# Performance work log

Hardware: AMD Instinct MI355X
Metric: run time of the kernel (lower is better)

## Reference

```python
import jax, jax.numpy as jnp
import numpy as np
import math

PHI = (1.0 + math.sqrt(5.0)) / 2.0
B, S, E, H = 4, 1024, 1024, 16
D = E // H  # head_dim = 64


def setup_inputs() -> dict:
    key = jax.random.key(0)
    ks = jax.random.split(key, 16)
    w = 0.02  # stand-in for xavier(gain=1/phi); math is init-agnostic
    inp = {
        "query": jax.random.normal(ks[0], (B, S, E), jnp.float32),
        "key": jax.random.normal(ks[1], (B, S, E), jnp.float32),
        "value": jax.random.normal(ks[2], (B, S, E), jnp.float32),
        "consciousness_levels": jax.random.uniform(ks[3], (B, S), jnp.float32),
        # causal mask, broadcast over batch and heads
        "attn_mask": jnp.tril(jnp.ones((S, S), bool))[None, None],
        # projection weights stored [in, out] (torch Linear applies x @ W.T)
        "Wq": jax.random.normal(ks[4], (E, E), jnp.float32) * w,
        "bq": jnp.zeros((E,), jnp.float32),
        "Wk": jax.random.normal(ks[5], (E, E), jnp.float32) * w,
        "bk": jnp.zeros((E,), jnp.float32),
        "Wv": jax.random.normal(ks[6], (E, E), jnp.float32) * w,
        "bv": jnp.zeros((E,), jnp.float32),
        "Wo": jax.random.normal(ks[7], (E, E), jnp.float32) * w,
        "bo": jnp.zeros((E,), jnp.float32),
        "Wc": jax.random.normal(ks[8], (E, H), jnp.float32) * w,
        "bc": jnp.zeros((H,), jnp.float32),
        # phi_bias[h] = (h+1)/phi**(h+1), shape [H,1,1] as in _init_weights
        "phi_bias": jnp.array([(h + 1) / PHI ** (h + 1) for h in range(H)],
                               jnp.float32).reshape(H, 1, 1),
    }
    return inp


def reference(query, key, value, consciousness_levels, attn_mask,
              Wq, bq, Wk, bk, Wv, bv, Wo, bo, Wc, bc, phi_bias):
    # project and split heads: [B,S,E] -> [B,H,S,D]
    q = (query @ Wq + bq).reshape(B, S, H, D).transpose(0, 2, 1, 3)
    k = (key @ Wk + bk).reshape(B, S, H, D).transpose(0, 2, 1, 3)
    v = (value @ Wv + bv).reshape(B, S, H, D).transpose(0, 2, 1, 3)

    inv_scale = 1.0 / (math.sqrt(D) * math.sqrt(PHI))  # phi-scaled 1/sqrt(d)
    scores = jnp.einsum('bhqd,bhkd->bhqk', q, k) * inv_scale
    scores = scores + phi_bias[None]                   # per-head additive bias
    scores = jnp.where(attn_mask, scores, -jnp.inf)
    attn = jax.nn.softmax(scores, axis=-1)             # [B,H,S,S]

    # consciousness reweighting + second softmax (faithful to original)
    cw = jax.nn.softmax(query @ Wc + bc, axis=-1)      # [B,S,H]
    cw = cw.transpose(0, 2, 1)[..., None]              # [B,H,S,1]
    cb = consciousness_levels[:, None, :, None]        # [B,1,S,1]
    attn = jax.nn.softmax(attn * (1.0 + cb * cw), axis=-1)

    ctx = jnp.einsum('bhqk,bhkd->bhqd', attn, v)
    ctx = ctx.transpose(0, 2, 1, 3).reshape(B, S, E)
    out = ctx @ Wo + bo
    return out, attn
```

## Files before the change

kernel.cpp:

```cpp
#include <hip/hip_runtime.h>
#include <stdint.h>

#define B_ 4
#define S_ 1024
#define E_ 1024
#define H_ 16
#define D_ 64

typedef unsigned short u16;
typedef short s16x8 __attribute__((ext_vector_type(8)));
typedef unsigned short u16x8 __attribute__((ext_vector_type(8)));
typedef unsigned short u16x4 __attribute__((ext_vector_type(4)));
typedef float f32x4 __attribute__((ext_vector_type(4)));

__device__ __forceinline__ u16 f2bf(float f) {
    union { float f; uint32_t i; } x; x.f = f;
    uint32_t r = (x.i + 0x7FFFu + ((x.i >> 16) & 1u)) >> 16;
    return (u16)r;
}

__device__ __forceinline__ float wave_sum(float v) {
    #pragma unroll
    for (int o = 32; o; o >>= 1) v += __shfl_xor(v, o);
    return v;
}

template<int BM, int BN, int EPI, bool AF32>
__global__ __launch_bounds__(256, 2)
void gemm_bt(const void* __restrict__ Avoid, int lda, long sA,
             const u16* __restrict__ BT, int ldb, long sB,
             const float* __restrict__ bias,
             void* __restrict__ Cvoid, int ldc, int K)
{
    constexpr int BK = 32;
    constexpr int FM = BM / 32;
    constexpr int FN = BN / 32;
    constexpr int NAF = (BM * BK) / 4 / 256;
    constexpr int NAB = (BM * BK) / 8 / 256;
    constexpr int NB  = (BN * BK) / 8 / 256;
    __shared__ __attribute__((aligned(16))) u16 As[BM * BK];
    __shared__ __attribute__((aligned(16))) u16 Bs[BN * BK];

    const int t = threadIdx.x;
    const int lane = t & 63;
    const int wave = t >> 6;
    const int wr = wave >> 1, wc = wave & 1;
    const int z = blockIdx.z;
    const int m0 = blockIdx.y * BM, n0 = blockIdx.x * BN;

    const float* Af = ((const float*)Avoid) + (size_t)z * sA;
    const u16*  Ab  = ((const u16*)Avoid) + (size_t)z * sA;
    const u16*  Bp  = BT + (size_t)z * sB;

    f32x4 ra[NAF];
    u16x8 rab[NAB];
    u16x8 rb[NB];

    auto loadA = [&](int k0) {
        if constexpr (AF32) {
            #pragma unroll
            for (int i = 0; i < NAF; i++) {
                int c = i * 256 + t, row = c >> 3, cc = c & 7;
                ra[i] = *(const f32x4*)(Af + (size_t)(m0 + row) * lda + k0 + cc * 4);
            }
        } else {
            #pragma unroll
            for (int i = 0; i < NAB; i++) {
                int c = i * 256 + t, row = c >> 2, cc = c & 3;
                rab[i] = *(const u16x8*)(Ab + (size_t)(m0 + row) * lda + k0 + cc * 8);
            }
        }
    };
    auto loadB = [&](int k0) {
        #pragma unroll
        for (int i = 0; i < NB; i++) {
            int c = i * 256 + t, row = c >> 2, cc = c & 3;
            rb[i] = *(const u16x8*)(Bp + (size_t)(n0 + row) * ldb + k0 + cc * 8);
        }
    };
    auto storeLDS = [&]() {
        if constexpr (AF32) {
            #pragma unroll
            for (int i = 0; i < NAF; i++) {
                int c = i * 256 + t;
                u16x4 o;
                o[0] = f2bf(ra[i][0]); o[1] = f2bf(ra[i][1]);
                o[2] = f2bf(ra[i][2]); o[3] = f2bf(ra[i][3]);
                *(u16x4*)(As + c * 4) = o;
            }
        } else {
            #pragma unroll
            for (int i = 0; i < NAB; i++) {
                int c = i * 256 + t;
                *(u16x8*)(As + c * 8) = rab[i];
            }
        }
        #pragma unroll
        for (int i = 0; i < NB; i++) {
            int c = i * 256 + t;
            *(u16x8*)(Bs + c * 8) = rb[i];
        }
    };

    f32x4 acc[FM][FN];
    #pragma unroll
    for (int i = 0; i < FM; i++)
        #pragma unroll
        for (int j = 0; j < FN; j++)
            acc[i][j] = (f32x4){0.f, 0.f, 0.f, 0.f};

    const int al = lane & 15;
    const int aq = lane >> 4;

    loadA(0); loadB(0);
    for (int k0 = 0; k0 < K; k0 += BK) {
        __syncthreads();
        storeLDS();
        __syncthreads();
        if (k0 + BK < K) { loadA(k0 + BK); loadB(k0 + BK); }

        s16x8 af[FM], bf[FN];
        #pragma unroll
        for (int i = 0; i < FM; i++)
            af[i] = *(const s16x8*)(As + ((wr * FM + i) * 16 + al) * BK + aq * 8);
        #pragma unroll
        for (int j = 0; j < FN; j++)
            bf[j] = *(const s16x8*)(Bs + ((wc * FN + j) * 16 + al) * BK + aq * 8);
        #pragma unroll
        for (int i = 0; i < FM; i++)
            #pragma unroll
            for (int j = 0; j < FN; j++)
                acc[i][j] = __builtin_amdgcn_mfma_f32_16x16x32_bf16(af[i], bf[j], acc[i][j], 0, 0, 0);
    }

    float* Cf = (float*)Cvoid;
    u16*   Cb = (u16*)Cvoid;
    #pragma unroll
    for (int i = 0; i < FM; i++) {
        #pragma unroll
        for (int j = 0; j < FN; j++) {
            const int col = n0 + (wc * FN + j) * 16 + al;
            const float bv = bias[col];
            #pragma unroll
            for (int r = 0; r < 4; r++) {
                const int row = m0 + (wr * FM + i) * 16 + aq * 4 + r;
                float v = acc[i][j][r] + bv;
                if (EPI == 0) {
                    Cf[(size_t)row * ldc + col] = v;
                } else if (EPI == 1) {
                    int b = row >> 10, s = row & 1023, h = col >> 6, d = col & 63;
                    Cb[((size_t)((b * H_ + h) * S_ + s)) * D_ + d] = f2bf(v);
                } else {
                    int b = row >> 10, s = row & 1023, h = col >> 6, d = col & 63;
                    Cb[((size_t)((b * H_ + h) * D_ + d)) * S_ + s] = f2bf(v);
                }
            }
        }
    }
}

__global__ __launch_bounds__(256)
void cons_k(const float* __restrict__ query, const float* __restrict__ Wc,
            const float* __restrict__ bc, const float* __restrict__ cl,
            float* __restrict__ mws)
{
    const int t = threadIdx.x, lane = t & 63, wave = t >> 6;
    const int r = blockIdx.x * 4 + wave;
    const float* qrow = query + (size_t)r * E_;
    float acc[H_];
    #pragma unroll
    for (int c = 0; c < H_; c++) acc[c] = 0.f;
    for (int e = lane; e < E_; e += 64) {
        float qv = qrow[e];
        const float* wp = Wc + e * H_;
        f32x4 w0 = *(const f32x4*)(wp);
        f32x4 w1 = *(const f32x4*)(wp + 4);
        f32x4 w2 = *(const f32x4*)(wp + 8);
        f32x4 w3 = *(const f32x4*)(wp + 12);
        #pragma unroll
        for (int c = 0; c < 4; c++) {
            acc[c]      += qv * w0[c];
            acc[4 + c]  += qv * w1[c];
            acc[8 + c]  += qv * w2[c];
            acc[12 + c] += qv * w3[c];
        }
    }
    #pragma unroll
    for (int c = 0; c < H_; c++) acc[c] = wave_sum(acc[c]);
    float mx = -3e38f;
    #pragma unroll
    for (int c = 0; c < H_; c++) { acc[c] += bc[c]; mx = fmaxf(mx, acc[c]); }
    float se = 0.f;
    #pragma unroll
    for (int c = 0; c < H_; c++) { acc[c] = __expf(acc[c] - mx); se += acc[c]; }
    if (lane < H_) {
        float mycw = 0.f;
        #pragma unroll
        for (int c = 0; c < H_; c++) if (lane == c) mycw = acc[c];
        mycw /= se;
        int b = r >> 10, s = r & 1023;
        float clv = cl[r];
        mws[((size_t)(b * H_ + lane)) * S_ + s] = 1.f + clv * mycw;
    }
}

#define LD_ 1028
__global__ __launch_bounds__(256, 2)
void attn_fused(const u16* __restrict__ q_ws, const u16* __restrict__ k_ws,
                const u16* __restrict__ vt_ws, const float* __restrict__ mws,
                float* __restrict__ attn_out, u16* __restrict__ ctx_ws,
                float alpha)
{
    __shared__ __attribute__((aligned(16))) float sc[16 * LD_];
    __shared__ float red[16 * 16];
    __shared__ float rowmax[16], scl1[16], invz[16];

    const int t = threadIdx.x, lane = t & 63, w = t >> 6;
    const int al = lane & 15, aq = lane >> 4;
    const int bh = blockIdx.y;
    const int q0 = blockIdx.x * 16;

    const u16* Qp = q_ws + ((size_t)bh * S_ + q0) * D_;
    const u16* Kp = k_ws + (size_t)bh * S_ * D_ + (size_t)(w * 256) * D_;
    const u16* Vp = vt_ws + (size_t)bh * D_ * S_;

    s16x8 qf0 = *(const s16x8*)(Qp + (size_t)al * D_ + aq * 8);
    s16x8 qf1 = *(const s16x8*)(Qp + (size_t)al * D_ + 32 + aq * 8);
    #pragma unroll
    for (int mf = 0; mf < 16; mf++) {
        const u16* kr = Kp + (size_t)(mf * 16 + al) * D_ + aq * 8;
        s16x8 kf0 = *(const s16x8*)(kr);
        s16x8 kf1 = *(const s16x8*)(kr + 32);
        f32x4 a0 = (f32x4){0.f, 0.f, 0.f, 0.f};
        a0 = __builtin_amdgcn_mfma_f32_16x16x32_bf16(kf0, qf0, a0, 0, 0, 0);
        a0 = __builtin_amdgcn_mfma_f32_16x16x32_bf16(kf1, qf1, a0, 0, 0, 0);
        const int kc = w * 256 + mf * 16 + aq * 4;
        f32x4 o;
        #pragma unroll
        for (int j = 0; j < 4; j++) o[j] = a0[j] * alpha;
        *(f32x4*)(sc + (size_t)al * LD_ + kc) = o;
    }
    __syncthreads();

    const int row = t & 15, cg = t >> 4;
    const int q = q0 + row;
    float* rp = sc + (size_t)row * LD_ + cg * 4;

    float mx = -3e38f;
    #pragma unroll 4
    for (int k = 0; k < 16; k++) {
        f32x4 v = *(const f32x4*)(rp + k * 64);
        const int cb = cg * 4 + k * 64;
        #pragma unroll
        for (int j = 0; j < 4; j++)
            if (cb + j <= q) mx = fmaxf(mx, v[j]);
    }
    red[cg * 16 + row] = mx;
    __syncthreads();
    if (t < 16) {
        float m = red[t];
        #pragma unroll
        for (int c = 1; c < 16; c++) m = fmaxf(m, red[c * 16 + t]);
        rowmax[t] = m;
    }
    __syncthreads();

    const float mxr = rowmax[row];
    float s1 = 0.f;
    #pragma unroll 4
    for (int k = 0; k < 16; k++) {
        f32x4 v = *(const f32x4*)(rp + k * 64);
        const int cb = cg * 4 + k * 64;
        f32x4 o;
        #pragma unroll
        for (int j = 0; j < 4; j++) {
            float e = (cb + j <= q) ? __expf(v[j] - mxr) : 0.f;
            o[j] = e; s1 += e;
        }
        *(f32x4*)(rp + k * 64) = o;
    }
    red[cg * 16 + row] = s1;
    __syncthreads();
    if (t < 16) {
        float s = 0.f;
        #pragma unroll
        for (int c = 0; c < 16; c++) s += red[c * 16 + t];
        scl1[t] = mws[(size_t)bh * S_ + q0 + t] / s;
    }
    __syncthreads();

    const float sl = scl1[row];
    float s2 = 0.f;
    #pragma unroll 4
    for (int k = 0; k < 16; k++) {
        f32x4 v = *(const f32x4*)(rp + k * 64);
        const int cb = cg * 4 + k * 64;
        f32x4 o;
        #pragma unroll
        for (int j = 0; j < 4; j++) {
            float e = (cb + j <= q) ? __expf(v[j] * sl) : 1.f;
            o[j] = e; s2 += e;
        }
        *(f32x4*)(rp + k * 64) = o;
    }
    red[cg * 16 + row] = s2;
    __syncthreads();
    if (t < 16) {
        float s = 0.f;
        #pragma unroll
        for (int c = 0; c < 16; c++) s += red[c * 16 + t];
        invz[t] = 1.f / s;
    }
    __syncthreads();

    f32x4 pa[4];
    #pragma unroll
    for (int nf = 0; nf < 4; nf++) pa[nf] = (f32x4){0.f, 0.f, 0.f, 0.f};
    #pragma unroll
    for (int ks = 0; ks < 8; ks++) {
        const int kb = w * 256 + ks * 32;
        const float* ap = sc + (size_t)al * LD_ + kb + aq * 8;
        f32x4 x0 = *(const f32x4*)(ap);
        f32x4 x1 = *(const f32x4*)(ap + 4);
        s16x8 af;
        af[0] = (short)f2bf(x0[0]); af[1] = (short)f2bf(x0[1]);
        af[2] = (short)f2bf(x0[2]); af[3] = (short)f2bf(x0[3]);
        af[4] = (short)f2bf(x1[0]); af[5] = (short)f2bf(x1[1]);
        af[6] = (short)f2bf(x1[2]); af[7] = (short)f2bf(x1[3]);
        #pragma unroll
        for (int nf = 0; nf < 4; nf++) {
            s16x8 bf = *(const s16x8*)(Vp + (size_t)(nf * 16 + al) * S_ + kb + aq * 8);
            pa[nf] = __builtin_amdgcn_mfma_f32_16x16x32_bf16(af, bf, pa[nf], 0, 0, 0);
        }
    }

    float* ao = attn_out + (size_t)bh * S_ * S_ + (size_t)q0 * S_;
    #pragma unroll
    for (int rr = 0; rr < 4; rr++) {
        const int r2 = w * 4 + rr;
        const float iz = invz[r2];
        #pragma unroll
        for (int k2 = 0; k2 < 4; k2++) {
            f32x4 v = *(const f32x4*)(sc + (size_t)r2 * LD_ + k2 * 256 + lane * 4);
            f32x4 o;
            #pragma unroll
            for (int j = 0; j < 4; j++) o[j] = v[j] * iz;
            *(f32x4*)(ao + (size_t)r2 * S_ + k2 * 256 + lane * 4) = o;
        }
    }
    __syncthreads();

    {
        float* dp = sc + w * (64 * 20);
        #pragma unroll
        for (int nf = 0; nf < 4; nf++)
            *(f32x4*)(dp + (size_t)(nf * 16 + al) * 20 + aq * 4) = pa[nf];
    }
    __syncthreads();
    {
        const int r5 = t >> 4, d0 = (t & 15) * 4;
        const float iz = invz[r5];
        float o[4] = {0.f, 0.f, 0.f, 0.f};
        #pragma unroll
        for (int ww = 0; ww < 4; ww++) {
            const float* rp5 = sc + ww * (64 * 20) + r5;
            #pragma unroll
            for (int dd = 0; dd < 4; dd++) o[dd] += rp5[(size_t)(d0 + dd) * 20];
        }
        u16x4 ob;
        #pragma unroll
        for (int dd = 0; dd < 4; dd++) ob[dd] = f2bf(o[dd] * iz);
        const int b = bh >> 4, h = bh & 15;
        *(u16x4*)(ctx_ws + ((size_t)(b * S_ + q0 + r5)) * E_ + h * 64 + d0) = ob;
    }
}

__global__ __launch_bounds__(256)
void transpose4_k(const float* __restrict__ W0, const float* __restrict__ W1,
                  const float* __restrict__ W2, const float* __restrict__ W3,
                  u16* __restrict__ out)
{
    __shared__ float tile[32][33];
    const int zz = blockIdx.z;
    const float* in = (zz == 0) ? W0 : (zz == 1) ? W1 : (zz == 2) ? W2 : W3;
    u16* o = out + (size_t)zz * E_ * E_;
    const int t = threadIdx.x;
    const int tx = t & 31, ty = t >> 5;
    const int bx = blockIdx.x * 32, by = blockIdx.y * 32;
    #pragma unroll
    for (int i = 0; i < 32; i += 8)
        tile[ty + i][tx] = in[(size_t)(by + ty + i) * E_ + bx + tx];
    __syncthreads();
    #pragma unroll
    for (int i = 0; i < 32; i += 8)
        o[(size_t)(bx + ty + i) * E_ + by + tx] = f2bf(tile[tx][ty + i]);
}

extern "C" void kernel_launch(void* const* d_in, const int* in_sizes, int n_in,
                              void* d_out, int out_size, void* d_ws, size_t ws_size,
                              hipStream_t stream)
{
    const float* query = (const float*)d_in[0];
    const float* key_  = (const float*)d_in[1];
    const float* value = (const float*)d_in[2];
    const float* cl    = (const float*)d_in[3];
    const float* Wq = (const float*)d_in[5];
    const float* bq = (const float*)d_in[6];
    const float* Wk = (const float*)d_in[7];
    const float* bk = (const float*)d_in[8];
    const float* Wv = (const float*)d_in[9];
    const float* bv = (const float*)d_in[10];
    const float* Wo = (const float*)d_in[11];
    const float* bo = (const float*)d_in[12];
    const float* Wc = (const float*)d_in[13];
    const float* bc = (const float*)d_in[14];

    float* out  = (float*)d_out;
    float* attn = out + (size_t)B_ * S_ * E_;

    u16* q_ws   = (u16*)d_ws;
    u16* k_ws   = q_ws  + (size_t)B_ * S_ * E_;
    u16* vt_ws  = k_ws  + (size_t)B_ * S_ * E_;
    u16* ctx_ws = vt_ws + (size_t)B_ * S_ * E_;
    u16* wt     = ctx_ws + (size_t)B_ * S_ * E_;
    float* mws  = (float*)(wt + (size_t)4 * E_ * E_);

    const float inv_scale = 0.09826892502579689f;
    dim3 blk(256);

    transpose4_k<<<dim3(32, 32, 4), blk, 0, stream>>>(Wq, Wk, Wv, Wo, wt);

    cons_k<<<B_ * S_ / 4, blk, 0, stream>>>(query, Wc, bc, cl, mws);

    gemm_bt<128, 64, 1, true><<<dim3(16, 32, 1), blk, 0, stream>>>(
        query, E_, 0, wt, E_, 0, bq, q_ws, 0, E_);
    gemm_bt<128, 64, 1, true><<<dim3(16, 32, 1), blk, 0, stream>>>(
        key_, E_, 0, wt + (size_t)E_ * E_, E_, 0, bk, k_ws, 0, E_);
    gemm_bt<128, 64, 2, true><<<dim3(16, 32, 1), blk, 0, stream>>>(
        value, E_, 0, wt + (size_t)2 * E_ * E_, E_, 0, bv, vt_ws, 0, E_);

    attn_fused<<<dim3(S_ / 16, B_ * H_), blk, 0, stream>>>(
        q_ws, k_ws, vt_ws, mws, attn, ctx_ws, inv_scale);

    gemm_bt<128, 64, 0, false><<<dim3(16, 32, 1), blk, 0, stream>>>(
        ctx_ws, E_, 0, wt + (size_t)3 * E_ * E_, E_, 0, bo, out, E_, E_);
}
```

Measured before the change: 589.2 us.

## Pre-convert inputs to bf16, batch QKV GEMM with direct-to-LDS loads, widen attention block

A separate kernel converts query, key and value to bf16 once, writing them into the not-yet-used attention output buffer as scratch. The three projection GEMMs become one launch with 128x128 tiles that load global memory straight into LDS via global_load_lds, replacing the register-staged fp32 loads. The attention kernel moves to 512 threads, each wave owning 128 keys, and keeps the scores in registers between the softmax passes instead of writing them back to shared memory. The GEMM loop drops its register prefetch and waits on each load before computing, so memory and MFMA work overlap less within a block.

Result: faster. 556.8 us (-5.5%).

```diff
diff --git a/kernel.cpp b/kernel.cpp
--- a/kernel.cpp
+++ b/kernel.cpp
@@ -11,6 +11,7 @@
 typedef short s16x8 __attribute__((ext_vector_type(8)));
 typedef unsigned short u16x8 __attribute__((ext_vector_type(8)));
 typedef unsigned short u16x4 __attribute__((ext_vector_type(4)));
+typedef unsigned short u16x2 __attribute__((ext_vector_type(2)));
 typedef float f32x4 __attribute__((ext_vector_type(4)));
 
 __device__ __forceinline__ u16 f2bf(float f) {
@@ -25,137 +26,159 @@
     return v;
 }
 
-template<int BM, int BN, int EPI, bool AF32>
-__global__ __launch_bounds__(256, 2)
-void gemm_bt(const void* __restrict__ Avoid, int lda, long sA,
-             const u16* __restrict__ BT, int ldb, long sB,
-             const float* __restrict__ bias,
-             void* __restrict__ Cvoid, int ldc, int K)
-{
-    constexpr int BK = 32;
-    constexpr int FM = BM / 32;
-    constexpr int FN = BN / 32;
-    constexpr int NAF = (BM * BK) / 4 / 256;
-    constexpr int NAB = (BM * BK) / 8 / 256;
-    constexpr int NB  = (BN * BK) / 8 / 256;
-    __shared__ __attribute__((aligned(16))) u16 As[BM * BK];
-    __shared__ __attribute__((aligned(16))) u16 Bs[BN * BK];
-
-    const int t = threadIdx.x;
-    const int lane = t & 63;
-    const int wave = t >> 6;
-    const int wr = wave >> 1, wc = wave & 1;
-    const int z = blockIdx.z;
-    const int m0 = blockIdx.y * BM, n0 = blockIdx.x * BN;
-
-    const float* Af = ((const float*)Avoid) + (size_t)z * sA;
-    const u16*  Ab  = ((const u16*)Avoid) + (size_t)z * sA;
-    const u16*  Bp  = BT + (size_t)z * sB;
-
-    f32x4 ra[NAF];
-    u16x8 rab[NAB];
-    u16x8 rb[NB];
-
-    auto loadA = [&](int k0) {
-        if constexpr (AF32) {
-            #pragma unroll
-            for (int i = 0; i < NAF; i++) {
-                int c = i * 256 + t, row = c >> 3, cc = c & 7;
-                ra[i] = *(const f32x4*)(Af + (size_t)(m0 + row) * lda + k0 + cc * 4);
-            }
-        } else {
-            #pragma unroll
-            for (int i = 0; i < NAB; i++) {
-                int c = i * 256 + t, row = c >> 2, cc = c & 3;
-                rab[i] = *(const u16x8*)(Ab + (size_t)(m0 + row) * lda + k0 + cc * 8);
-            }
-        }
-    };
-    auto loadB = [&](int k0) {
-        #pragma unroll
-        for (int i = 0; i < NB; i++) {
-            int c = i * 256 + t, row = c >> 2, cc = c & 3;
-            rb[i] = *(const u16x8*)(Bp + (size_t)(n0 + row) * ldb + k0 + cc * 8);
-        }
-    };
-    auto storeLDS = [&]() {
-        if constexpr (AF32) {
-            #pragma unroll
-            for (int i = 0; i < NAF; i++) {
-                int c = i * 256 + t;
-                u16x4 o;
-                o[0] = f2bf(ra[i][0]); o[1] = f2bf(ra[i][1]);
-                o[2] = f2bf(ra[i][2]); o[3] = f2bf(ra[i][3]);
-                *(u16x4*)(As + c * 4) = o;
-            }
-        } else {
-            #pragma unroll
-            for (int i = 0; i < NAB; i++) {
-                int c = i * 256 + t;
-                *(u16x8*)(As + c * 8) = rab[i];
-            }
-        }
-        #pragma unroll
-        for (int i = 0; i < NB; i++) {
-            int c = i * 256 + t;
-            *(u16x8*)(Bs + c * 8) = rb[i];
-        }
-    };
-
-    f32x4 acc[FM][FN];
-    #pragma unroll
-    for (int i = 0; i < FM; i++)
+__device__ __forceinline__ void gload16(const u16* g, u16* l) {
+    __builtin_amdgcn_global_load_lds(
+        (const __attribute__((address_space(1))) void*)g,
+        (__attribute__((address_space(3))) void*)l, 16, 0, 0);
+}
+
+template<int BM, int BN>
+__device__ __forceinline__ void gemm_core(
+    const u16* __restrict__ Ab, int lda,
+    const u16* __restrict__ Bp, int ldb,
+    int m0, int n0, int K,
+    u16* As, u16* Bs, f32x4 (&acc)[BM / 32][BN / 32])
+{
+    constexpr int FM = BM / 32, FN = BN / 32;
+    constexpr int ACH = BM / 64;
+    constexpr int BCH = BN / 64;
+    const int t = threadIdx.x, lane = t & 63, w = t >> 6;
+    const int wr = w >> 1, wc = w & 1, al = lane & 15, aq = lane >> 4;
+
+    for (int k0 = 0; k0 < K; k0 += 32) {
+        #pragma unroll
+        for (int i = 0; i < ACH; i++) {
+            const int c = i * 256 + w * 64 + lane;
+            gload16(Ab + (size_t)(m0 + (c >> 2)) * lda + k0 + (c & 3) * 8,
+                    As + (size_t)(i * 256 + w * 64) * 8);
+        }
+        #pragma unroll
+        for (int i = 0; i < BCH; i++) {
+            const int c = i * 256 + w * 64 + lane;
+            gload16(Bp + (size_t)(n0 + (c >> 2)) * ldb + k0 + (c & 3) * 8,
+                    Bs + (size_t)(i * 256 + w * 64) * 8);
+        }
+        asm volatile("s_waitcnt vmcnt(0)" ::: "memory");
+        __syncthreads();
+
+        s16x8 af[FM], bf[FN];
+        #pragma unroll
+        for (int i = 0; i < FM; i++)
+            af[i] = *(const s16x8*)(As + ((wr * FM + i) * 16 + al) * 32 + aq * 8);
         #pragma unroll
         for (int j = 0; j < FN; j++)
-            acc[i][j] = (f32x4){0.f, 0.f, 0.f, 0.f};
-
-    const int al = lane & 15;
-    const int aq = lane >> 4;
-
-    loadA(0); loadB(0);
-    for (int k0 = 0; k0 < K; k0 += BK) {
-        __syncthreads();
-        storeLDS();
-        __syncthreads();
-        if (k0 + BK < K) { loadA(k0 + BK); loadB(k0 + BK); }
-
-        s16x8 af[FM], bf[FN];
-        #pragma unroll
-        for (int i = 0; i < FM; i++)
-            af[i] = *(const s16x8*)(As + ((wr * FM + i) * 16 + al) * BK + aq * 8);
-        #pragma unroll
-        for (int j = 0; j < FN; j++)
-            bf[j] = *(const s16x8*)(Bs + ((wc * FN + j) * 16 + al) * BK + aq * 8);
+            bf[j] = *(const s16x8*)(Bs + ((wc * FN + j) * 16 + al) * 32 + aq * 8);
         #pragma unroll
         for (int i = 0; i < FM; i++)
             #pragma unroll
             for (int j = 0; j < FN; j++)
                 acc[i][j] = __builtin_amdgcn_mfma_f32_16x16x32_bf16(af[i], bf[j], acc[i][j], 0, 0, 0);
-    }
-
-    float* Cf = (float*)Cvoid;
-    u16*   Cb = (u16*)Cvoid;
-    #pragma unroll
-    for (int i = 0; i < FM; i++) {
-        #pragma unroll
-        for (int j = 0; j < FN; j++) {
-            const int col = n0 + (wc * FN + j) * 16 + al;
-            const float bv = bias[col];
+        __syncthreads();
+    }
+}
+
+__global__ __launch_bounds__(256, 3)
+void gemm_qkv(const u16* __restrict__ qbf, const u16* __restrict__ kbf,
+              const u16* __restrict__ vbf, const u16* __restrict__ wt,
+              const float* __restrict__ bq, const float* __restrict__ bk,
+              const float* __restrict__ bv,
+              u16* __restrict__ q_ws, u16* __restrict__ k_ws,
+              u16* __restrict__ vt_ws)
+{
+    __shared__ __attribute__((aligned(16))) u16 As[128 * 32];
+    __shared__ __attribute__((aligned(16))) u16 Bs[128 * 32];
+    const int z = blockIdx.z;
+    const u16* Ab = (z == 0) ? qbf : (z == 1) ? kbf : vbf;
+    const u16* Bp = wt + (size_t)z * E_ * E_;
+    const float* bias = (z == 0) ? bq : (z == 1) ? bk : bv;
+    u16* Cb = (z == 0) ? q_ws : (z == 1) ? k_ws : vt_ws;
+    const int m0 = blockIdx.y * 128, n0 = blockIdx.x * 128;
+
+    f32x4 acc[4][4];
+    #pragma unroll
+    for (int i = 0; i < 4; i++)
+        #pragma unroll
+        for (int j = 0; j < 4; j++)
+            acc[i][j] = (f32x4){0.f, 0.f, 0.f, 0.f};
+
+    gemm_core<128, 128>(Ab, E_, Bp, E_, m0, n0, E_, As, Bs, acc);
+
+    const int t = threadIdx.x, lane = t & 63, w = t >> 6;
+    const int wr = w >> 1, wc = w & 1, al = lane & 15, aq = lane >> 4;
+    #pragma unroll
+    for (int i = 0; i < 4; i++) {
+        #pragma unroll
+        for (int j = 0; j < 4; j++) {
+            const int col = n0 + (wc * 4 + j) * 16 + al;
+            const float bvv = bias[col];
             #pragma unroll
             for (int r = 0; r < 4; r++) {
-                const int row = m0 + (wr * FM + i) * 16 + aq * 4 + r;
-                float v = acc[i][j][r] + bv;
-                if (EPI == 0) {
-                    Cf[(size_t)row * ldc + col] = v;
-                } else if (EPI == 1) {
-                    int b = row >> 10, s = row & 1023, h = col >> 6, d = col & 63;
-                    Cb[((size_t)((b * H_ + h) * S_ + s)) * D_ + d] = f2bf(v);
-                } else {
-                    int b = row >> 10, s = row & 1023, h = col >> 6, d = col & 63;
-                    Cb[((size_t)((b * H_ + h) * D_ + d)) * S_ + s] = f2bf(v);
-                }
+                const int row = m0 + (wr * 4 + i) * 16 + aq * 4 + r;
+                const float vv = acc[i][j][r] + bvv;
+                const int b = row >> 10, s = row & 1023, h = col >> 6, d = col & 63;
+                if (z < 2)
+                    Cb[((size_t)((b * H_ + h) * S_ + s)) * D_ + d] = f2bf(vv);
+                else
+                    Cb[((size_t)((b * H_ + h) * D_ + d)) * S_ + s] = f2bf(vv);
             }
         }
+    }
+}
+
+__global__ __launch_bounds__(256, 3)
+void gemm_o(const u16* __restrict__ ctx, const u16* __restrict__ wt3,
+            const float* __restrict__ bo, float* __restrict__ out)
+{
+    __shared__ __attribute__((aligned(16))) u16 As[128 * 32];
+    __shared__ __attribute__((aligned(16))) u16 Bs[64 * 32];
+    const int m0 = blockIdx.y * 128, n0 = blockIdx.x * 64;
+
+    f32x4 acc[4][2];
+    #pragma unroll
+    for (int i = 0; i < 4; i++)
+        #pragma unroll
+        for (int j = 0; j < 2; j++)
+            acc[i][j] = (f32x4){0.f, 0.f, 0.f, 0.f};
+
+    gemm_core<128, 64>(ctx, E_, wt3, E_, m0, n0, E_, As, Bs, acc);
+
+    const int t = threadIdx.x, lane = t & 63, w = t >> 6;
+    const int wr = w >> 1, wc = w & 1, al = lane & 15, aq = lane >> 4;
+    #pragma unroll
+    for (int i = 0; i < 4; i++) {
+        #pragma unroll
+        for (int j = 0; j < 2; j++) {
+            const int col = n0 + (wc * 2 + j) * 16 + al;
+            const float bvv = bo[col];
+            #pragma unroll
+            for (int r = 0; r < 4; r++) {
+                const int row = m0 + (wr * 4 + i) * 16 + aq * 4 + r;
+                out[(size_t)row * E_ + col] = acc[i][j][r] + bvv;
+            }
+        }
+    }
+}
+
+__device__ __forceinline__ void cvt8(const float* __restrict__ src,
+                                     u16* __restrict__ dst, int i) {
+    f32x4 a = *(const f32x4*)(src + (size_t)i * 8);
+    f32x4 b = *(const f32x4*)(src + (size_t)i * 8 + 4);
+    u16x8 o;
+    o[0] = f2bf(a[0]); o[1] = f2bf(a[1]); o[2] = f2bf(a[2]); o[3] = f2bf(a[3]);
+    o[4] = f2bf(b[0]); o[5] = f2bf(b[1]); o[6] = f2bf(b[2]); o[7] = f2bf(b[3]);
+    *(u16x8*)(dst + (size_t)i * 8) = o;
+}
+
+__global__ __launch_bounds__(256)
+void cvt3_k(const float* __restrict__ q, const float* __restrict__ k,
+            const float* __restrict__ v, u16* __restrict__ oq,
+            u16* __restrict__ ok, u16* __restrict__ ov)
+{
+    const int n = B_ * S_ * E_ / 8;
+    for (int i = blockIdx.x * 256 + threadIdx.x; i < n; i += gridDim.x * 256) {
+        cvt8(q, oq, i);
+        cvt8(k, ok, i);
+        cvt8(v, ov, i);
     }
 }
 
@@ -205,14 +228,14 @@
 }
 
 #define LD_ 1028
-__global__ __launch_bounds__(256, 2)
+__global__ __launch_bounds__(512, 4)
 void attn_fused(const u16* __restrict__ q_ws, const u16* __restrict__ k_ws,
                 const u16* __restrict__ vt_ws, const float* __restrict__ mws,
                 float* __restrict__ attn_out, u16* __restrict__ ctx_ws,
                 float alpha)
 {
     __shared__ __attribute__((aligned(16))) float sc[16 * LD_];
-    __shared__ float red[16 * 16];
+    __shared__ float red[32 * 16];
     __shared__ float rowmax[16], scl1[16], invz[16];
 
     const int t = threadIdx.x, lane = t & 63, w = t >> 6;
@@ -221,20 +244,20 @@
     const int q0 = blockIdx.x * 16;
 
     const u16* Qp = q_ws + ((size_t)bh * S_ + q0) * D_;
-    const u16* Kp = k_ws + (size_t)bh * S_ * D_ + (size_t)(w * 256) * D_;
+    const u16* Kp = k_ws + ((size_t)bh * S_ + w * 128) * D_;
     const u16* Vp = vt_ws + (size_t)bh * D_ * S_;
 
     s16x8 qf0 = *(const s16x8*)(Qp + (size_t)al * D_ + aq * 8);
     s16x8 qf1 = *(const s16x8*)(Qp + (size_t)al * D_ + 32 + aq * 8);
     #pragma unroll
-    for (int mf = 0; mf < 16; mf++) {
+    for (int mf = 0; mf < 8; mf++) {
         const u16* kr = Kp + (size_t)(mf * 16 + al) * D_ + aq * 8;
         s16x8 kf0 = *(const s16x8*)(kr);
         s16x8 kf1 = *(const s16x8*)(kr + 32);
         f32x4 a0 = (f32x4){0.f, 0.f, 0.f, 0.f};
         a0 = __builtin_amdgcn_mfma_f32_16x16x32_bf16(kf0, qf0, a0, 0, 0, 0);
         a0 = __builtin_amdgcn_mfma_f32_16x16x32_bf16(kf1, qf1, a0, 0, 0, 0);
-        const int kc = w * 256 + mf * 16 + aq * 4;
+        const int kc = w * 128 + mf * 16 + aq * 4;
         f32x4 o;
         #pragma unroll
         for (int j = 0; j < 4; j++) o[j] = a0[j] * alpha;
@@ -246,69 +269,66 @@
     const int q = q0 + row;
     float* rp = sc + (size_t)row * LD_ + cg * 4;
 
+    f32x4 sv[8];
     float mx = -3e38f;
-    #pragma unroll 4
-    for (int k = 0; k < 16; k++) {
-        f32x4 v = *(const f32x4*)(rp + k * 64);
-        const int cb = cg * 4 + k * 64;
+    #pragma unroll
+    for (int k = 0; k < 8; k++) {
+        sv[k] = *(const f32x4*)(rp + k * 128);
+        const int cb = cg * 4 + k * 128;
         #pragma unroll
         for (int j = 0; j < 4; j++)
-            if (cb + j <= q) mx = fmaxf(mx, v[j]);
+            if (cb + j <= q) mx = fmaxf(mx, sv[k][j]);
     }
     red[cg * 16 + row] = mx;
     __syncthreads();
     if (t < 16) {
         float m = red[t];
         #pragma unroll
-        for (int c = 1; c < 16; c++) m = fmaxf(m, red[c * 16 + t]);
+        for (int c = 1; c < 32; c++) m = fmaxf(m, red[c * 16 + t]);
         rowmax[t] = m;
     }
     __syncthreads();
 
     const float mxr = rowmax[row];
     float s1 = 0.f;
-    #pragma unroll 4
-    for (int k = 0; k < 16; k++) {
-        f32x4 v = *(const f32x4*)(rp + k * 64);
-        const int cb = cg * 4 + k * 64;
-        f32x4 o;
+    #pragma unroll
+    for (int k = 0; k < 8; k++) {
+        const int cb = cg * 4 + k * 128;
         #pragma unroll
         for (int j = 0; j < 4; j++) {
-            float e = (cb + j <= q) ? __expf(v[j] - mxr) : 0.f;
-            o[j] = e; s1 += e;
-        }
-        *(f32x4*)(rp + k * 64) = o;
+            float e = (cb + j <= q) ? __expf(sv[k][j] - mxr) : 0.f;
+            sv[k][j] = e; s1 += e;
+        }
     }
     red[cg * 16 + row] = s1;
     __syncthreads();
     if (t < 16) {
         float s = 0.f;
         #pragma unroll
-        for (int c = 0; c < 16; c++) s += red[c * 16 + t];
+        for (int c = 0; c < 32; c++) s += red[c * 16 + t];
         scl1[t] = mws[(size_t)bh * S_ + q0 + t] / s;
     }
     __syncthreads();
 
     const float sl = scl1[row];
     float s2 = 0.f;
-    #pragma unroll 4
-    for (int k = 0; k < 16; k++) {
-        f32x4 v = *(const f32x4*)(rp + k * 64);
-        const int cb = cg * 4 + k * 64;
+    #pragma unroll
+    for (int k = 0; k < 8; k++) {
+        const int cb = cg * 4 + k * 128;
         f32x4 o;
         #pragma unroll
         for (int j = 0; j < 4; j++) {
-            float e = (cb + j <= q) ? __expf(v[j] * sl) : 1.f;
+            float e = (cb + j <= q) ? __expf(sv[k][j] * sl) : 1.f;
             o[j] = e; s2 += e;
         }
-        *(f32x4*)(rp + k * 64) = o;
+        *(f32x4*)(rp + k * 128) = o;
     }
     red[cg * 16 + row] = s2;
     __syncthreads();
     if (t < 16) {
         float s = 0.f;
         #pragma unroll
-        for (int c = 0; c < 16; c++) s += red[c * 16 + t];
+        for (int c = 0; c < 32; c++) s += red[c * 16 + t];
         invz[t] = 1.f / s;
     }
     __syncthreads();
@@ -317,8 +337,8 @@
     #pragma unroll
     for (int nf = 0; nf < 4; nf++) pa[nf] = (f32x4){0.f, 0.f, 0.f, 0.f};
     #pragma unroll
-    for (int ks = 0; ks < 8; ks++) {
-        const int kb = w * 256 + ks * 32;
+    for (int ks = 0; ks < 4; ks++) {
+        const int kb = w * 128 + ks * 32;
         const float* ap = sc + (size_t)al * LD_ + kb + aq * 8;
         f32x4 x0 = *(const f32x4*)(ap);
         f32x4 x1 = *(const f32x4*)(ap + 4);
@@ -329,15 +349,15 @@
         af[6] = (short)f2bf(x1[2]); af[7] = (short)f2bf(x1[3]);
         #pragma unroll
         for (int nf = 0; nf < 4; nf++) {
-            s16x8 bf = *(const s16x8*)(Vp + (size_t)(nf * 16 + al) * S_ + kb + aq * 8);
-            pa[nf] = __builtin_amdgcn_mfma_f32_16x16x32_bf16(af, bf, pa[nf], 0, 0, 0);
+            s16x8 bfv = *(const s16x8*)(Vp + (size_t)(nf * 16 + al) * S_ + kb + aq * 8);
+            pa[nf] = __builtin_amdgcn_mfma_f32_16x16x32_bf16(af, bfv, pa[nf], 0, 0, 0);
         }
     }
 
     float* ao = attn_out + (size_t)bh * S_ * S_ + (size_t)q0 * S_;
     #pragma unroll
-    for (int rr = 0; rr < 4; rr++) {
-        const int r2 = w * 4 + rr;
+    for (int rr = 0; rr < 2; rr++) {
+        const int r2 = w * 2 + rr;
         const float iz = invz[r2];
         #pragma unroll
         for (int k2 = 0; k2 < 4; k2++) {
@@ -358,20 +378,21 @@
     }
     __syncthreads();
     {
-        const int r5 = t >> 4, d0 = (t & 15) * 4;
+        const int r5 = t >> 5, d0 = (t & 31) * 2;
         const float iz = invz[r5];
-        float o[4] = {0.f, 0.f, 0.f, 0.f};
-        #pragma unroll
-        for (int ww = 0; ww < 4; ww++) {
+        float o0 = 0.f, o1 = 0.f;
+        #pragma unroll
+        for (int ww = 0; ww < 8; ww++) {
             const float* rp5 = sc + ww * (64 * 20) + r5;
-            #pragma unroll
-            for (int dd = 0; dd < 4; dd++) o[dd] += rp5[(size_t)(d0 + dd) * 20];
-        }
-        u16x4 ob;
-        #pragma unroll
-        for (int dd = 0; dd < 4; dd++) ob[dd] = f2bf(o[dd] * iz);
+            o0 += rp5[(size_t)d0 * 20];
+            o1 += rp5[(size_t)(d0 + 1) * 20];
+        }
         const int b = bh >> 4, h = bh & 15;
-        *(u16x4*)(ctx_ws + ((size_t)(b * S_ + q0 + r5)) * E_ + h * 64 + d0) = ob;
+        u16* cp = ctx_ws + ((size_t)(b * S_ + q0 + r5)) * E_ + h * 64 + d0;
+        u16x2 ob;
+        ob[0] = f2bf(o0 * iz);
+        ob[1] = f2bf(o1 * iz);
+        *(u16x2*)cp = ob;
     }
 }
 
@@ -425,23 +446,25 @@
     u16* wt     = ctx_ws + (size_t)B_ * S_ * E_;
     float* mws  = (float*)(wt + (size_t)4 * E_ * E_);
 
+    u16* qbf = (u16*)attn;
+    u16* kbf = qbf + (size_t)B_ * S_ * E_;
+    u16* vbf = kbf + (size_t)B_ * S_ * E_;
+
     const float inv_scale = 0.09826892502579689f;
     dim3 blk(256);
 
     transpose4_k<<<dim3(32, 32, 4), blk, 0, stream>>>(Wq, Wk, Wv, Wo, wt);
 
+    cvt3_k<<<2048, blk, 0, stream>>>(query, key_, value, qbf, kbf, vbf);
+
     cons_k<<<B_ * S_ / 4, blk, 0, stream>>>(query, Wc, bc, cl, mws);
 
-    gemm_bt<128, 64, 1, true><<<dim3(16, 32, 1), blk, 0, stream>>>(
-        query, E_, 0, wt, E_, 0, bq, q_ws, 0, E_);
-    gemm_bt<128, 64, 1, true><<<dim3(16, 32, 1), blk, 0, stream>>>(
-        key_, E_, 0, wt + (size_t)E_ * E_, E_, 0, bk, k_ws, 0, E_);
-    gemm_bt<128, 64, 2, true><<<dim3(16, 32, 1), blk, 0, stream>>>(
-        value, E_, 0, wt + (size_t)2 * E_ * E_, E_, 0, bv, vt_ws, 0, E_);
-
-    attn_fused<<<dim3(S_ / 16, B_ * H_), blk, 0, stream>>>(
+    gemm_qkv<<<dim3(8, 32, 3), blk, 0, stream>>>(
+        qbf, kbf, vbf, wt, bq, bk, bv, q_ws, k_ws, vt_ws);
+
+    attn_fused<<<dim3(S_ / 16, B_ * H_), dim3(512), 0, stream>>>(
         q_ws, k_ws, vt_ws, mws, attn, ctx_ws, inv_scale);
 
-    gemm_bt<128, 64, 0, false><<<dim3(16, 32, 1), blk, 0, stream>>>(
-        ctx_ws, E_, 0, wt + (size_t)3 * E_ * E_, E_, 0, bo, out, E_, E_);
-}
+    gemm_o<<<dim3(16, 32, 1), blk, 0, stream>>>(
+        ctx_ws, wt + (size_t)3 * E_ * E_, bo, out);
+}
```
